# Kernel tuning notes

Measured on AMD Instinct MI355X. Metric: run time of the kernel, lower is better.

The kernel has to match this reference:

```python
import jax, jax.numpy as jnp
import numpy as np

B, H, S, D = 2, 16, 2048, 64
SCALE = D ** -0.5  # head_dim^-0.5 with dim=1024, num_heads=16


def setup_inputs() -> dict:
    key = jax.random.key(0)
    kq, kk, kv = jax.random.split(key, 3)
    q = jax.random.normal(kq, (B, H, S, D), dtype=jnp.float32)
    k = jax.random.normal(kk, (B, H, S, D), dtype=jnp.float32)
    v = jax.random.normal(kv, (B, H, S, D), dtype=jnp.float32)
    # causal mask, broadcastable over batch and heads; 0 -> masked
    mask = jnp.tril(jnp.ones((S, S), dtype=jnp.int32))[None, None]
    return {"q": q, "k": k, "v": v, "mask": mask}


def reference(q, k, v, mask):
    # scores: [B, H, S, S]
    scores = jnp.einsum("bhqd,bhkd->bhqk", q, k) * SCALE
    scores = jnp.where(mask == 0, jnp.float32(-jnp.inf), scores)
    attn_weights = jax.nn.softmax(scores, axis=-1)
    # dropout p=0 / eval mode -> identity
    attn_output = jnp.einsum("bhqk,bhkd->bhqd", attn_weights, v)
    return attn_output, attn_weights
```

## Files before the change

kernel.cpp:

```cpp
#include <hip/hip_runtime.h>


#define S_LEN 2048
#define HD 64
#define NHEADS 32
#define NQT 32
#define ATT_SCALE 0.125f

typedef __bf16 bf16x8 __attribute__((ext_vector_type(8)));
typedef unsigned short u16x8 __attribute__((ext_vector_type(8)));
typedef float f32x4 __attribute__((ext_vector_type(4)));

__device__ __forceinline__ unsigned short f2bf(float f) {
  unsigned int u = __builtin_bit_cast(unsigned int, f);
  u += 0x7fffu + ((u >> 16) & 1u);
  return (unsigned short)(u >> 16);
}
__device__ __forceinline__ bf16x8 frag16(const unsigned short* p) {
  uint4 u = *reinterpret_cast<const uint4*>(p);
  return __builtin_bit_cast(bf16x8, u);
}
__device__ __forceinline__ bf16x8 cvt8(const float* p) {
  const float4 a = *reinterpret_cast<const float4*>(p);
  const float4 b = *reinterpret_cast<const float4*>(p + 4);
  u16x8 r;
  r[0] = f2bf(a.x); r[1] = f2bf(a.y); r[2] = f2bf(a.z); r[3] = f2bf(a.w);
  r[4] = f2bf(b.x); r[5] = f2bf(b.y); r[6] = f2bf(b.z); r[7] = f2bf(b.w);
  return __builtin_bit_cast(bf16x8, r);
}
__device__ __forceinline__ bf16x8 load8(const void* base, size_t off, bool isf32) {
  if (isf32) return cvt8(reinterpret_cast<const float*>(base) + off);
  return frag16(reinterpret_cast<const unsigned short*>(base) + off);
}
__device__ __forceinline__ bool sniff_f32(const void* q) {
  const int lane = threadIdx.x & 63;
  const unsigned int w = reinterpret_cast<const unsigned int*>(q)[lane];
  const unsigned int le = (w >> 7) & 0xFFu;
  const bool okb = (le == 0u) || (le >= 100u && le <= 140u);
  return __popcll(__ballot(okb)) < 32;
}

__global__ __launch_bounds__(256) void prep_kernel(
    const void* __restrict__ q, const void* __restrict__ k, const void* __restrict__ v,
    unsigned short* __restrict__ wq, unsigned short* __restrict__ wk,
    unsigned short* __restrict__ wv) {
  __shared__ __align__(16) unsigned short T[HD][72];
  const int tid = threadIdx.x;
  if (blockIdx.x >= 1024) {
    const bool isf32 = sniff_f32(q);
    const size_t i = ((size_t)(blockIdx.x - 1024) * 256 + tid) * 8;
    bf16x8 a = load8(q, i, isf32);
    *reinterpret_cast<uint4*>(wq + i) = __builtin_bit_cast(uint4, a);
    bf16x8 b = load8(k, i, isf32);
    *reinterpret_cast<uint4*>(wk + i) = __builtin_bit_cast(uint4, b);
    return;
  }
  const bool isf32 = sniff_f32(v);
  const int head = blockIdx.x & (NHEADS - 1);
  const int tt = blockIdx.x >> 5;
  const int r = tid >> 2;
  const int dc = (tid & 3) << 4;
  const size_t off = ((size_t)head * S_LEN + (tt << 6) + r) * HD + dc;
  const bf16x8 x0 = load8(v, off, isf32);
  const bf16x8 x1 = load8(v, off + 8, isf32);
  const u16x8 e0 = __builtin_bit_cast(u16x8, x0);
  const u16x8 e1 = __builtin_bit_cast(u16x8, x1);
#pragma unroll
  for (int e = 0; e < 8; ++e) { T[dc + e][r] = e0[e]; T[dc + 8 + e][r] = e1[e]; }
  __syncthreads();
  const int d = tid >> 2;
  const int tc = (tid & 3) << 4;
  const uint4 o0 = *reinterpret_cast<const uint4*>(&T[d][tc]);
  const uint4 o1 = *reinterpret_cast<const uint4*>(&T[d][tc + 8]);
  unsigned short* dst = wv + (((size_t)(head * NQT + tt) * HD + d) << 6) + tc;
  *reinterpret_cast<uint4*>(dst) = o0;
  *reinterpret_cast<uint4*>(dst + 8) = o1;
}

template <bool WS>
__global__ __launch_bounds__(256, 4) void attn_kernel(
    const void* __restrict__ q, const void* __restrict__ kk, const void* __restrict__ vv,
    const unsigned short* __restrict__ wq, const unsigned short* __restrict__ wk,
    const unsigned short* __restrict__ wv,
    float* __restrict__ out_o, float* __restrict__ out_w) {
  __shared__ __align__(16) unsigned short Vt[WS ? 8 : 2 * HD * 72];

  const int blk = blockIdx.x;
  const int head = blk & (NHEADS - 1);
  const int qt = (NQT - 1) - (blk >> 5);
  const int tid = threadIdx.x;
  const int lane = tid & 63;
  const int wave = tid >> 6;
  const int q0 = qt << 6;
  const int r0 = q0 + (wave << 4);
  const int l15 = lane & 15;
  const int quad = lane >> 4;

  bool isf32 = true;
  if constexpr (!WS) isf32 = sniff_f32(q);

  const size_t qb = (size_t)head * S_LEN * HD;
  float* Wh = out_w + (size_t)head * S_LEN * S_LEN;

  {
    const int c0 = (qt + 1) << 6;
    const int nz4 = (S_LEN - c0) >> 2;
    const int row = tid >> 2;
    const f32x4 z = {0.f, 0.f, 0.f, 0.f};
    f32x4* wrow = reinterpret_cast<f32x4*>(Wh + (size_t)(q0 + row) * S_LEN + c0);
    for (int c = tid & 3; c < nz4; c += 4) __builtin_nontemporal_store(z, wrow + c);
  }

  const size_t qoff = qb + (size_t)(r0 + l15) * HD + (quad << 3);
  bf16x8 qa0, qa1;
  if constexpr (WS) { qa0 = frag16(wq + qoff); qa1 = frag16(wq + qoff + 32); }
  else              { qa0 = load8(q, qoff, isf32); qa1 = load8(q, qoff + 32, isf32); }

  const int krow_l = ((l15 >> 2) << 3) + (l15 & 3);
  auto ldk = [&](int kt, int f) -> bf16x8 {
    const int s = f >> 1;
    const int row = (kt << 6) + krow_l + ((s & 1) << 2) + ((s >> 1) << 5);
    const size_t o = qb + (size_t)row * HD + (quad << 3) + ((f & 1) << 5);
    if constexpr (WS) return frag16(wk + o);
    else return load8(kk, o, isf32);
  };
  const int kib_base = (quad << 3);
  const int qi = r0 + l15;

  float lsum = 0.f;
  {
    bf16x8 kc[8], kn[8];
#pragma unroll
    for (int f = 0; f < 8; ++f) kc[f] = ldk(0, f);
    for (int kt = 0; kt <= qt; ++kt) {
      if (kt < qt) {
#pragma unroll
        for (int f = 0; f < 8; ++f) kn[f] = ldk(kt + 1, f);
      }
      if (kt == qt) {
#pragma unroll
        for (int s = 0; s < 4; ++s) {
          f32x4 acc = {0.f, 0.f, 0.f, 0.f};
          acc = __builtin_amdgcn_mfma_f32_16x16x32_bf16(kc[2 * s], qa0, acc, 0, 0, 0);
          acc = __builtin_amdgcn_mfma_f32_16x16x32_bf16(kc[2 * s + 1], qa1, acc, 0, 0, 0);
          const int kib = (kt << 6) + kib_base + ((s & 1) << 2) + ((s >> 1) << 5);
#pragma unroll
          for (int r = 0; r < 4; ++r)
            lsum += (kib + r <= qi) ? __expf(acc[r] * ATT_SCALE) : 0.f;
        }
      } else {
#pragma unroll
        for (int s = 0; s < 4; ++s) {
          f32x4 acc = {0.f, 0.f, 0.f, 0.f};
          acc = __builtin_amdgcn_mfma_f32_16x16x32_bf16(kc[2 * s], qa0, acc, 0, 0, 0);
          acc = __builtin_amdgcn_mfma_f32_16x16x32_bf16(kc[2 * s + 1], qa1, acc, 0, 0, 0);
#pragma unroll
          for (int r = 0; r < 4; ++r) lsum += __expf(acc[r] * ATT_SCALE);
        }
#pragma unroll
        for (int f = 0; f < 8; ++f) kc[f] = kn[f];
      }
    }
  }
  lsum += __shfl_xor(lsum, 16);
  lsum += __shfl_xor(lsum, 32);
  const float inv_l = 1.0f / lsum;

  const f32x4 vzero = {0.f, 0.f, 0.f, 0.f};
  f32x4 oacc[4] = {vzero, vzero, vzero, vzero};

  if constexpr (WS) {
    const unsigned short* wvh = wv + ((size_t)(head * NQT) << 12);
    for (int kt = 0; kt <= qt; ++kt) {
      const bool last = (kt == qt);
      bf16x8 kf[8];
#pragma unroll
      for (int f = 0; f < 8; ++f) kf[f] = ldk(kt, f);
      bf16x8 vf[8];
      {
        const unsigned short* tb = wvh + ((size_t)kt << 12);
#pragma unroll
        for (int nc2 = 0; nc2 < 4; ++nc2) {
          const unsigned short* rp = tb + (((nc2 << 4) + l15) << 6) + (quad << 3);
          vf[2 * nc2] = frag16(rp);
          vf[2 * nc2 + 1] = frag16(rp + 32);
        }
      }

      float pb[4][4];
#pragma unroll
      for (int s = 0; s < 4; ++s) {
        f32x4 acc = {0.f, 0.f, 0.f, 0.f};
        acc = __builtin_amdgcn_mfma_f32_16x16x32_bf16(kf[2 * s], qa0, acc, 0, 0, 0);
        acc = __builtin_amdgcn_mfma_f32_16x16x32_bf16(kf[2 * s + 1], qa1, acc, 0, 0, 0);
        const int kib = (kt << 6) + kib_base + ((s & 1) << 2) + ((s >> 1) << 5);
        f32x4 pv;
#pragma unroll
        for (int r = 0; r < 4; ++r) {
          float p = __expf(acc[r] * ATT_SCALE) * inv_l;
          if (last) p = (kib + r <= qi) ? p : 0.f;
          pb[s][r] = p;
          pv[r] = p;
        }
        __builtin_nontemporal_store(
            pv, reinterpret_cast<f32x4*>(Wh + (size_t)qi * S_LEN + kib));
      }
      u16x8 a0, a1;
#pragma unroll
      for (int r = 0; r < 4; ++r) {
        a0[r] = f2bf(pb[0][r]); a0[4 + r] = f2bf(pb[1][r]);
        a1[r] = f2bf(pb[2][r]); a1[4 + r] = f2bf(pb[3][r]);
      }
      const bf16x8 pa0 = __builtin_bit_cast(bf16x8, a0);
      const bf16x8 pa1 = __builtin_bit_cast(bf16x8, a1);
#pragma unroll
      for (int nc2 = 0; nc2 < 4; ++nc2) {
        oacc[nc2] = __builtin_amdgcn_mfma_f32_16x16x32_bf16(pa0, vf[2 * nc2], oacc[nc2], 0, 0, 0);
        oacc[nc2] = __builtin_amdgcn_mfma_f32_16x16x32_bf16(pa1, vf[2 * nc2 + 1], oacc[nc2], 0, 0, 0);
      }
    }
  } else {
    const int ftr1 = tid >> 3, fdc = (tid & 7) << 3;
    const int ftr2 = (tid + 256) >> 3;
    bf16x8 fv0, fv1;
    auto vload = [&](int kt) {
      fv0 = load8(vv, qb + (size_t)((kt << 6) + ftr1) * HD + fdc, isf32);
      fv1 = load8(vv, qb + (size_t)((kt << 6) + ftr2) * HD + fdc, isf32);
    };
    auto vstage = [&](int buf) {
      const u16x8 s0 = __builtin_bit_cast(u16x8, fv0);
      const u16x8 s1 = __builtin_bit_cast(u16x8, fv1);
      const int tb1 = ftr1 >> 3, tl1 = ftr1 & 7;
      const int tb2 = ftr2 >> 3, tl2 = ftr2 & 7;
      unsigned short* Vb = &Vt[buf * HD * 72];
#pragma unroll
      for (int e = 0; e < 8; ++e) {
        const int d = fdc + e;
        Vb[d * 72 + (((tb1 ^ (d >> 3)) << 3) | tl1)] = s0[e];
        Vb[d * 72 + (((tb2 ^ (d >> 3)) << 3) | tl2)] = s1[e];
      }
    };
    vload(0);
    vstage(0);
    __syncthreads();
    for (int kt = 0; kt <= qt; ++kt) {
      const bool last = (kt == qt);
      bf16x8 kf[8];
#pragma unroll
      for (int f = 0; f < 8; ++f) kf[f] = ldk(kt, f);
      if (!last) vload(kt + 1);

      float pb[4][4];
#pragma unroll
      for (int s = 0; s < 4; ++s) {
        f32x4 acc = {0.f, 0.f, 0.f, 0.f};
        acc = __builtin_amdgcn_mfma_f32_16x16x32_bf16(kf[2 * s], qa0, acc, 0, 0, 0);
        acc = __builtin_amdgcn_mfma_f32_16x16x32_bf16(kf[2 * s + 1], qa1, acc, 0, 0, 0);
        const int kib = (kt << 6) + kib_base + ((s & 1) << 2) + ((s >> 1) << 5);
        f32x4 pv;
#pragma unroll
        for (int r = 0; r < 4; ++r) {
          float p = __expf(acc[r] * ATT_SCALE) * inv_l;
          if (last) p = (kib + r <= qi) ? p : 0.f;
          pb[s][r] = p;
          pv[r] = p;
        }
        __builtin_nontemporal_store(
            pv, reinterpret_cast<f32x4*>(Wh + (size_t)qi * S_LEN + kib));
      }
      u16x8 a0, a1;
#pragma unroll
      for (int r = 0; r < 4; ++r) {
        a0[r] = f2bf(pb[0][r]); a0[4 + r] = f2bf(pb[1][r]);
        a1[r] = f2bf(pb[2][r]); a1[4 + r] = f2bf(pb[3][r]);
      }
      const bf16x8 pa0 = __builtin_bit_cast(bf16x8, a0);
      const bf16x8 pa1 = __builtin_bit_cast(bf16x8, a1);
      const unsigned short* Vc = &Vt[(kt & 1) * HD * 72];
#pragma unroll
      for (int nc2 = 0; nc2 < 4; ++nc2) {
        const int n = (nc2 << 4) + l15;
        const unsigned short* vbp = Vc + n * 72;
        const int nb = n >> 3;
        const bf16x8 v0 = frag16(vbp + ((quad ^ nb) << 3));
        const bf16x8 v1 = frag16(vbp + (((4 + quad) ^ nb) << 3));
        oacc[nc2] = __builtin_amdgcn_mfma_f32_16x16x32_bf16(pa0, v0, oacc[nc2], 0, 0, 0);
        oacc[nc2] = __builtin_amdgcn_mfma_f32_16x16x32_bf16(pa1, v1, oacc[nc2], 0, 0, 0);
      }
      if (!last) {
        vstage((kt + 1) & 1);
        __syncthreads();
      }
    }
  }

#pragma unroll
  for (int nc2 = 0; nc2 < 4; ++nc2)
#pragma unroll
    for (int r = 0; r < 4; ++r)
      out_o[(size_t)(head * S_LEN + r0 + (quad << 2) + r) * HD + (nc2 << 4) + l15] =
          oacc[nc2][r];
}

extern "C" void kernel_launch(void* const* d_in, const int* in_sizes, int n_in,
                              void* d_out, int out_size, void* d_ws, size_t ws_size,
                              hipStream_t stream) {
  (void)in_sizes; (void)n_in; (void)out_size;
  const void* q = d_in[0];
  const void* k = d_in[1];
  const void* v = d_in[2];
  float* out = (float*)d_out;
  float* out_o = out;
  float* out_w = out + (size_t)NHEADS * S_LEN * HD;
  const size_t NE = (size_t)NHEADS * S_LEN * HD;
  if (d_ws && ws_size >= NE * 2 * 3) {
    unsigned short* wq = reinterpret_cast<unsigned short*>(d_ws);
    unsigned short* wk = wq + NE;
    unsigned short* wv = wk + NE;
    prep_kernel<<<dim3(1024 + NE / (256 * 8)), dim3(256), 0, stream>>>(q, k, v, wq, wk, wv);
    attn_kernel<true><<<dim3(NHEADS * NQT), dim3(256), 0, stream>>>(
        q, k, v, wq, wk, wv, out_o, out_w);
  } else {
    attn_kernel<false><<<dim3(NHEADS * NQT), dim3(256), 0, stream>>>(
        q, k, v, nullptr, nullptr, nullptr, out_o, out_w);
  }
}
```

Measured before the change: 779.6 us.

## Stage swizzled K/V tiles through double-buffered LDS in workspace attention kernel

The prep kernel now writes K and V in per-64-row tiles with an XOR swizzle. The workspace attention kernel cooperatively loads each K/V tile into double-buffered shared memory and reads MFMA fragments from LDS. Before, every wave loaded its own fragments straight from global memory. The change is meant to cut redundant global and L2 traffic across the four waves and to avoid LDS bank conflicts. It also moves zero-filling of the masked region to after the compute, and switches the attention-weight stores from nontemporal to regular stores, which may raise cache pollution and adds barriers per tile.

New measurement: 634.4 us. -18.6%, faster.

```diff
diff --git a/kernel.cpp b/kernel.cpp
--- a/kernel.cpp
+++ b/kernel.cpp
@@ -39,6 +39,7 @@
   const bool okb = (le == 0u) || (le >= 100u && le <= 140u);
   return __popcll(__ballot(okb)) < 32;
 }
+__device__ __forceinline__ int swz3(int r) { return (r & 3) | (((r >> 3) & 1) << 2); }
 
 __global__ __launch_bounds__(256) void prep_kernel(
     const void* __restrict__ q, const void* __restrict__ k, const void* __restrict__ v,
@@ -52,7 +53,14 @@
     bf16x8 a = load8(q, i, isf32);
     *reinterpret_cast<uint4*>(wq + i) = __builtin_bit_cast(uint4, a);
     bf16x8 b = load8(k, i, isf32);
-    *reinterpret_cast<uint4*>(wk + i) = __builtin_bit_cast(uint4, b);
+    const int d0 = (int)(i & 63);
+    const int t = (int)((i >> 6) & (S_LEN - 1));
+    const int head = (int)(i >> 17);
+    const int tl = t & 63;
+    const int sch = (d0 >> 3) ^ swz3(tl);
+    unsigned short* dst =
+        wk + (((size_t)(head << 5) + (t >> 6)) << 12) + tl * 64 + (sch << 3);
+    *reinterpret_cast<uint4*>(dst) = __builtin_bit_cast(uint4, b);
     return;
   }
   const bool isf32 = sniff_f32(v);
@@ -70,20 +78,20 @@
   __syncthreads();
   const int d = tid >> 2;
   const int tc = (tid & 3) << 4;
-  const uint4 o0 = *reinterpret_cast<const uint4*>(&T[d][tc]);
-  const uint4 o1 = *reinterpret_cast<const uint4*>(&T[d][tc + 8]);
-  unsigned short* dst = wv + (((size_t)(head * NQT + tt) * HD + d) << 6) + tc;
-  *reinterpret_cast<uint4*>(dst) = o0;
-  *reinterpret_cast<uint4*>(dst + 8) = o1;
-}
-
-template <bool WS>
-__global__ __launch_bounds__(256, 4) void attn_kernel(
-    const void* __restrict__ q, const void* __restrict__ kk, const void* __restrict__ vv,
+  const int c0 = tc >> 3;
+  unsigned short* base = wv + (((size_t)(head << 5) + tt) << 12) + d * 64;
+  *reinterpret_cast<uint4*>(base + ((c0 ^ swz3(d)) << 3)) =
+      *reinterpret_cast<const uint4*>(&T[d][tc]);
+  *reinterpret_cast<uint4*>(base + (((c0 + 1) ^ swz3(d)) << 3)) =
+      *reinterpret_cast<const uint4*>(&T[d][tc + 8]);
+}
+
+__global__ __launch_bounds__(256, 4) void attn_ws(
     const unsigned short* __restrict__ wq, const unsigned short* __restrict__ wk,
     const unsigned short* __restrict__ wv,
     float* __restrict__ out_o, float* __restrict__ out_w) {
-  __shared__ __align__(16) unsigned short Vt[WS ? 8 : 2 * HD * 72];
+  __shared__ __align__(16) unsigned short Kl[2][4096];
+  __shared__ __align__(16) unsigned short Vl[2][4096];
 
   const int blk = blockIdx.x;
   const int head = blk & (NHEADS - 1);
@@ -95,9 +103,157 @@
   const int r0 = q0 + (wave << 4);
   const int l15 = lane & 15;
   const int quad = lane >> 4;
-
-  bool isf32 = true;
-  if constexpr (!WS) isf32 = sniff_f32(q);
+  const int kswz = (l15 & 3) | (((l15 >> 2) & 1) << 2);
+  const int vswz = (l15 & 3) | (((l15 >> 3) & 1) << 2);
+  const int krow_l = ((l15 >> 2) << 3) + (l15 & 3);
+  const int qi = r0 + l15;
+
+  float* Wh = out_w + (size_t)head * S_LEN * S_LEN;
+  const unsigned short* wkh = wk + ((size_t)head << 17);
+  const unsigned short* wvh = wv + ((size_t)head << 17);
+
+  const size_t qoff = ((size_t)head << 17) + (size_t)(r0 + l15) * HD + (quad << 3);
+  const bf16x8 qa0 = frag16(wq + qoff);
+  const bf16x8 qa1 = frag16(wq + qoff + 32);
+
+  const int so = wave * 1024 + lane * 8;
+  uint4 sk0, sk1, sv0, sv1;
+  auto ldKg = [&](int kt) {
+    const unsigned short* p = wkh + ((size_t)kt << 12) + so;
+    sk0 = *reinterpret_cast<const uint4*>(p);
+    sk1 = *reinterpret_cast<const uint4*>(p + 512);
+  };
+  auto wrK = [&](int b) {
+    unsigned short* p = &Kl[b][so];
+    *reinterpret_cast<uint4*>(p) = sk0;
+    *reinterpret_cast<uint4*>(p + 512) = sk1;
+  };
+  auto ldVg = [&](int kt) {
+    const unsigned short* p = wvh + ((size_t)kt << 12) + so;
+    sv0 = *reinterpret_cast<const uint4*>(p);
+    sv1 = *reinterpret_cast<const uint4*>(p + 512);
+  };
+  auto wrV = [&](int b) {
+    unsigned short* p = &Vl[b][so];
+    *reinterpret_cast<uint4*>(p) = sv0;
+    *reinterpret_cast<uint4*>(p + 512) = sv1;
+  };
+
+  float lsum = 0.f;
+  ldKg(0); wrK(0); __syncthreads();
+  for (int kt = 0; kt <= qt; ++kt) {
+    if (kt < qt) ldKg(kt + 1);
+    const unsigned short* Kb = &Kl[kt & 1][0];
+#pragma unroll
+    for (int s = 0; s < 4; ++s) {
+      const int R = krow_l + ((s & 1) << 2) + ((s >> 1) << 5);
+      const unsigned short* rb = Kb + R * 64;
+      const bf16x8 k0 = frag16(rb + ((quad ^ kswz) << 3));
+      const bf16x8 k1 = frag16(rb + (((4 + quad) ^ kswz) << 3));
+      f32x4 acc = {0.f, 0.f, 0.f, 0.f};
+      acc = __builtin_amdgcn_mfma_f32_16x16x32_bf16(k0, qa0, acc, 0, 0, 0);
+      acc = __builtin_amdgcn_mfma_f32_16x16x32_bf16(k1, qa1, acc, 0, 0, 0);
+      if (kt == qt) {
+        const int kib = (kt << 6) + (quad << 3) + ((s & 1) << 2) + ((s >> 1) << 5);
+#pragma unroll
+        for (int r = 0; r < 4; ++r)
+          lsum += (kib + r <= qi) ? __expf(acc[r] * ATT_SCALE) : 0.f;
+      } else {
+#pragma unroll
+        for (int r = 0; r < 4; ++r) lsum += __expf(acc[r] * ATT_SCALE);
+      }
+    }
+    if (kt < qt) { wrK((kt + 1) & 1); __syncthreads(); }
+  }
+  lsum += __shfl_xor(lsum, 16);
+  lsum += __shfl_xor(lsum, 32);
+  const float inv_l = 1.0f / lsum;
+  __syncthreads();
+
+  const f32x4 vz = {0.f, 0.f, 0.f, 0.f};
+  f32x4 oacc[4] = {vz, vz, vz, vz};
+  ldKg(0); ldVg(0); wrK(0); wrV(0); __syncthreads();
+  for (int kt = 0; kt <= qt; ++kt) {
+    const bool last = (kt == qt);
+    if (!last) { ldKg(kt + 1); ldVg(kt + 1); }
+    const unsigned short* Kb = &Kl[kt & 1][0];
+    const unsigned short* Vb = &Vl[kt & 1][0];
+
+    float pb[4][4];
+#pragma unroll
+    for (int s = 0; s < 4; ++s) {
+      const int R = krow_l + ((s & 1) << 2) + ((s >> 1) << 5);
+      const unsigned short* rb = Kb + R * 64;
+      const bf16x8 k0 = frag16(rb + ((quad ^ kswz) << 3));
+      const bf16x8 k1 = frag16(rb + (((4 + quad) ^ kswz) << 3));
+      f32x4 acc = {0.f, 0.f, 0.f, 0.f};
+      acc = __builtin_amdgcn_mfma_f32_16x16x32_bf16(k0, qa0, acc, 0, 0, 0);
+      acc = __builtin_amdgcn_mfma_f32_16x16x32_bf16(k1, qa1, acc, 0, 0, 0);
+      const int kib = (kt << 6) + (quad << 3) + ((s & 1) << 2) + ((s >> 1) << 5);
+      f32x4 pv;
+#pragma unroll
+      for (int r = 0; r < 4; ++r) {
+        float p = __expf(acc[r] * ATT_SCALE) * inv_l;
+        if (last) p = (kib + r <= qi) ? p : 0.f;
+        pb[s][r] = p;
+        pv[r] = p;
+      }
+      *reinterpret_cast<f32x4*>(Wh + (size_t)qi * S_LEN + kib) = pv;
+    }
+    u16x8 a0, a1;
+#pragma unroll
+    for (int r = 0; r < 4; ++r) {
+      a0[r] = f2bf(pb[0][r]); a0[4 + r] = f2bf(pb[1][r]);
+      a1[r] = f2bf(pb[2][r]); a1[4 + r] = f2bf(pb[3][r]);
+    }
+    const bf16x8 pa0 = __builtin_bit_cast(bf16x8, a0);
+    const bf16x8 pa1 = __builtin_bit_cast(bf16x8, a1);
+#pragma unroll
+    for (int nc2 = 0; nc2 < 4; ++nc2) {
+      const unsigned short* rb = Vb + ((nc2 << 4) + l15) * 64;
+      const bf16x8 v0 = frag16(rb + ((quad ^ vswz) << 3));
+      const bf16x8 v1 = frag16(rb + (((4 + quad) ^ vswz) << 3));
+      oacc[nc2] = __builtin_amdgcn_mfma_f32_16x16x32_bf16(pa0, v0, oacc[nc2], 0, 0, 0);
+      oacc[nc2] = __builtin_amdgcn_mfma_f32_16x16x32_bf16(pa1, v1, oacc[nc2], 0, 0, 0);
+    }
+    if (!last) { wrK((kt + 1) & 1); wrV((kt + 1) & 1); __syncthreads(); }
+  }
+
+#pragma unroll
+  for (int nc2 = 0; nc2 < 4; ++nc2)
+#pragma unroll
+    for (int r = 0; r < 4; ++r)
+      out_o[(size_t)(head * S_LEN + r0 + (quad << 2) + r) * HD + (nc2 << 4) + l15] =
+          oacc[nc2][r];
+
+  {
+    const int c0 = (qt + 1) << 6;
+    const f32x4 z = {0.f, 0.f, 0.f, 0.f};
+#pragma unroll 1
+    for (int rr = 0; rr < 16; ++rr) {
+      float* rowp = Wh + (size_t)(r0 + rr) * S_LEN;
+      for (int c = c0 + (lane << 2); c < S_LEN; c += 256)
+        __builtin_nontemporal_store(z, reinterpret_cast<f32x4*>(rowp + c));
+    }
+  }
+}
+
+__global__ __launch_bounds__(256, 4) void attn_fb(
+    const void* __restrict__ q, const void* __restrict__ kk, const void* __restrict__ vv,
+    float* __restrict__ out_o, float* __restrict__ out_w) {
+  __shared__ __align__(16) unsigned short Vt[2 * HD * 72];
+
+  const int blk = blockIdx.x;
+  const int head = blk & (NHEADS - 1);
+  const int qt = (NQT - 1) - (blk >> 5);
+  const int tid = threadIdx.x;
+  const int lane = tid & 63;
+  const int wave = tid >> 6;
+  const int q0 = qt << 6;
+  const int r0 = q0 + (wave << 4);
+  const int l15 = lane & 15;
+  const int quad = lane >> 4;
+  const bool isf32 = sniff_f32(q);
 
   const size_t qb = (size_t)head * S_LEN * HD;
   float* Wh = out_w + (size_t)head * S_LEN * S_LEN;
@@ -108,21 +264,19 @@
     const int row = tid >> 2;
     const f32x4 z = {0.f, 0.f, 0.f, 0.f};
     f32x4* wrow = reinterpret_cast<f32x4*>(Wh + (size_t)(q0 + row) * S_LEN + c0);
-    for (int c = tid & 3; c < nz4; c += 4) __builtin_nontemporal_store(z, wrow + c);
+    for (int c = tid & 3; c < nz4; c += 4) wrow[c] = z;
   }
 
   const size_t qoff = qb + (size_t)(r0 + l15) * HD + (quad << 3);
-  bf16x8 qa0, qa1;
-  if constexpr (WS) { qa0 = frag16(wq + qoff); qa1 = frag16(wq + qoff + 32); }
-  else              { qa0 = load8(q, qoff, isf32); qa1 = load8(q, qoff + 32, isf32); }
+  const bf16x8 qa0 = load8(q, qoff, isf32);
+  const bf16x8 qa1 = load8(q, qoff + 32, isf32);
 
   const int krow_l = ((l15 >> 2) << 3) + (l15 & 3);
   auto ldk = [&](int kt, int f) -> bf16x8 {
     const int s = f >> 1;
     const int row = (kt << 6) + krow_l + ((s & 1) << 2) + ((s >> 1) << 5);
     const size_t o = qb + (size_t)row * HD + (quad << 3) + ((f & 1) << 5);
-    if constexpr (WS) return frag16(wk + o);
-    else return load8(kk, o, isf32);
+    return load8(kk, o, isf32);
   };
   const int kib_base = (quad << 3);
   const int qi = r0 + l15;
@@ -137,26 +291,17 @@
 #pragma unroll
         for (int f = 0; f < 8; ++f) kn[f] = ldk(kt + 1, f);
       }
-      if (kt == qt) {
-#pragma unroll
-        for (int s = 0; s < 4; ++s) {
-          f32x4 acc = {0.f, 0.f, 0.f, 0.f};
-          acc = __builtin_amdgcn_mfma_f32_16x16x32_bf16(kc[2 * s], qa0, acc, 0, 0, 0);
-          acc = __builtin_amdgcn_mfma_f32_16x16x32_bf16(kc[2 * s + 1], qa1, acc, 0, 0, 0);
-          const int kib = (kt << 6) + kib_base + ((s & 1) << 2) + ((s >> 1) << 5);
-#pragma unroll
-          for (int r = 0; r < 4; ++r)
-            lsum += (kib + r <= qi) ? __expf(acc[r] * ATT_SCALE) : 0.f;
-        }
-      } else {
-#pragma unroll
-        for (int s = 0; s < 4; ++s) {
-          f32x4 acc = {0.f, 0.f, 0.f, 0.f};
-          acc = __builtin_amdgcn_mfma_f32_16x16x32_bf16(kc[2 * s], qa0, acc, 0, 0, 0);
-          acc = __builtin_amdgcn_mfma_f32_16x16x32_bf16(kc[2 * s + 1], qa1, acc, 0, 0, 0);
-#pragma unroll
-          for (int r = 0; r < 4; ++r) lsum += __expf(acc[r] * ATT_SCALE);
-        }
+#pragma unroll
+      for (int s = 0; s < 4; ++s) {
+        f32x4 acc = {0.f, 0.f, 0.f, 0.f};
+        acc = __builtin_amdgcn_mfma_f32_16x16x32_bf16(kc[2 * s], qa0, acc, 0, 0, 0);
+        acc = __builtin_amdgcn_mfma_f32_16x16x32_bf16(kc[2 * s + 1], qa1, acc, 0, 0, 0);
+        const int kib = (kt << 6) + kib_base + ((s & 1) << 2) + ((s >> 1) << 5);
+#pragma unroll
+        for (int r = 0; r < 4; ++r)
+          lsum += (kt < qt || kib + r <= qi) ? __expf(acc[r] * ATT_SCALE) : 0.f;
+      }
+      if (kt < qt) {
 #pragma unroll
         for (int f = 0; f < 8; ++f) kc[f] = kn[f];
       }
@@ -166,131 +311,78 @@
   lsum += __shfl_xor(lsum, 32);
   const float inv_l = 1.0f / lsum;
 
-  const f32x4 vzero = {0.f, 0.f, 0.f, 0.f};
-  f32x4 oacc[4] = {vzero, vzero, vzero, vzero};
-
-  if constexpr (WS) {
-    const unsigned short* wvh = wv + ((size_t)(head * NQT) << 12);
-    for (int kt = 0; kt <= qt; ++kt) {
-      const bool last = (kt == qt);
-      bf16x8 kf[8];
-#pragma unroll
-      for (int f = 0; f < 8; ++f) kf[f] = ldk(kt, f);
-      bf16x8 vf[8];
-      {
-        const unsigned short* tb = wvh + ((size_t)kt << 12);
-#pragma unroll
-        for (int nc2 = 0; nc2 < 4; ++nc2) {
-          const unsigned short* rp = tb + (((nc2 << 4) + l15) << 6) + (quad << 3);
-          vf[2 * nc2] = frag16(rp);
-          vf[2 * nc2 + 1] = frag16(rp + 32);
-        }
-      }
-
-      float pb[4][4];
-#pragma unroll
-      for (int s = 0; s < 4; ++s) {
-        f32x4 acc = {0.f, 0.f, 0.f, 0.f};
-        acc = __builtin_amdgcn_mfma_f32_16x16x32_bf16(kf[2 * s], qa0, acc, 0, 0, 0);
-        acc = __builtin_amdgcn_mfma_f32_16x16x32_bf16(kf[2 * s + 1], qa1, acc, 0, 0, 0);
-        const int kib = (kt << 6) + kib_base + ((s & 1) << 2) + ((s >> 1) << 5);
-        f32x4 pv;
-#pragma unroll
-        for (int r = 0; r < 4; ++r) {
-          float p = __expf(acc[r] * ATT_SCALE) * inv_l;
-          if (last) p = (kib + r <= qi) ? p : 0.f;
-          pb[s][r] = p;
-          pv[r] = p;
-        }
-        __builtin_nontemporal_store(
-            pv, reinterpret_cast<f32x4*>(Wh + (size_t)qi * S_LEN + kib));
-      }
-      u16x8 a0, a1;
+  const f32x4 vz = {0.f, 0.f, 0.f, 0.f};
+  f32x4 oacc[4] = {vz, vz, vz, vz};
+
+  const int ftr1 = tid >> 3, fdc = (tid & 7) << 3;
+  const int ftr2 = (tid + 256) >> 3;
+  bf16x8 fv0, fv1;
+  auto vload = [&](int kt) {
+    fv0 = load8(vv, qb + (size_t)((kt << 6) + ftr1) * HD + fdc, isf32);
+    fv1 = load8(vv, qb + (size_t)((kt << 6) + ftr2) * HD + fdc, isf32);
+  };
+  auto vstage = [&](int buf) {
+    const u16x8 s0 = __builtin_bit_cast(u16x8, fv0);
+    const u16x8 s1 = __builtin_bit_cast(u16x8, fv1);
+    const int tb1 = ftr1 >> 3, tl1 = ftr1 & 7;
+    const int tb2 = ftr2 >> 3, tl2 = ftr2 & 7;
+    unsigned short* Vb = &Vt[buf * HD * 72];
+#pragma unroll
+    for (int e = 0; e < 8; ++e) {
+      const int d = fdc + e;
+      Vb[d * 72 + (((tb1 ^ (d >> 3)) << 3) | tl1)] = s0[e];
+      Vb[d * 72 + (((tb2 ^ (d >> 3)) << 3) | tl2)] = s1[e];
+    }
+  };
+  vload(0);
+  vstage(0);
+  __syncthreads();
+  for (int kt = 0; kt <= qt; ++kt) {
+    const bool last = (kt == qt);
+    bf16x8 kf[8];
+#pragma unroll
+    for (int f = 0; f < 8; ++f) kf[f] = ldk(kt, f);
+    if (!last) vload(kt + 1);
+
+    float pb[4][4];
+#pragma unroll
+    for (int s = 0; s < 4; ++s) {
+      f32x4 acc = {0.f, 0.f, 0.f, 0.f};
+      acc = __builtin_amdgcn_mfma_f32_16x16x32_bf16(kf[2 * s], qa0, acc, 0, 0, 0);
+      acc = __builtin_amdgcn_mfma_f32_16x16x32_bf16(kf[2 * s + 1], qa1, acc, 0, 0, 0);
+      const int kib = (kt << 6) + kib_base + ((s & 1) << 2) + ((s >> 1) << 5);
+      f32x4 pv;
 #pragma unroll
       for (int r = 0; r < 4; ++r) {
-        a0[r] = f2bf(pb[0][r]); a0[4 + r] = f2bf(pb[1][r]);
-        a1[r] = f2bf(pb[2][r]); a1[4 + r] = f2bf(pb[3][r]);
-      }
-      const bf16x8 pa0 = __builtin_bit_cast(bf16x8, a0);
-      const bf16x8 pa1 = __builtin_bit_cast(bf16x8, a1);
-#pragma unroll
-      for (int nc2 = 0; nc2 < 4; ++nc2) {
-        oacc[nc2] = __builtin_amdgcn_mfma_f32_16x16x32_bf16(pa0, vf[2 * nc2], oacc[nc2], 0, 0, 0);
-        oacc[nc2] = __builtin_amdgcn_mfma_f32_16x16x32_bf16(pa1, vf[2 * nc2 + 1], oacc[nc2], 0, 0, 0);
-      }
-    }
-  } else {
-    const int ftr1 = tid >> 3, fdc = (tid & 7) << 3;
-    const int ftr2 = (tid + 256) >> 3;
-    bf16x8 fv0, fv1;
-    auto vload = [&](int kt) {
-      fv0 = load8(vv, qb + (size_t)((kt << 6) + ftr1) * HD + fdc, isf32);
-      fv1 = load8(vv, qb + (size_t)((kt << 6) + ftr2) * HD + fdc, isf32);
-    };
-    auto vstage = [&](int buf) {
-      const u16x8 s0 = __builtin_bit_cast(u16x8, fv0);
-      const u16x8 s1 = __builtin_bit_cast(u16x8, fv1);
-      const int tb1 = ftr1 >> 3, tl1 = ftr1 & 7;
-      const int tb2 = ftr2 >> 3, tl2 = ftr2 & 7;
-      unsigned short* Vb = &Vt[buf * HD * 72];
-#pragma unroll
-      for (int e = 0; e < 8; ++e) {
-        const int d = fdc + e;
-        Vb[d * 72 + (((tb1 ^ (d >> 3)) << 3) | tl1)] = s0[e];
-        Vb[d * 72 + (((tb2 ^ (d >> 3)) << 3) | tl2)] = s1[e];
-      }
-    };
-    vload(0);
-    vstage(0);
-    __syncthreads();
-    for (int kt = 0; kt <= qt; ++kt) {
-      const bool last = (kt == qt);
-      bf16x8 kf[8];
-#pragma unroll
-      for (int f = 0; f < 8; ++f) kf[f] = ldk(kt, f);
-      if (!last) vload(kt + 1);
-
-      float pb[4][4];
-#pragma unroll
-      for (int s = 0; s < 4; ++s) {
-        f32x4 acc = {0.f, 0.f, 0.f, 0.f};
-        acc = __builtin_amdgcn_mfma_f32_16x16x32_bf16(kf[2 * s], qa0, acc, 0, 0, 0);
-        acc = __builtin_amdgcn_mfma_f32_16x16x32_bf16(kf[2 * s + 1], qa1, acc, 0, 0, 0);
-        const int kib = (kt << 6) + kib_base + ((s & 1) << 2) + ((s >> 1) << 5);
-        f32x4 pv;
-#pragma unroll
-        for (int r = 0; r < 4; ++r) {
-          float p = __expf(acc[r] * ATT_SCALE) * inv_l;
-          if (last) p = (kib + r <= qi) ? p : 0.f;
-          pb[s][r] = p;
-          pv[r] = p;
-        }
-        __builtin_nontemporal_store(
-            pv, reinterpret_cast<f32x4*>(Wh + (size_t)qi * S_LEN + kib));
-      }
-      u16x8 a0, a1;
-#pragma unroll
-      for (int r = 0; r < 4; ++r) {
-        a0[r] = f2bf(pb[0][r]); a0[4 + r] = f2bf(pb[1][r]);
-        a1[r] = f2bf(pb[2][r]); a1[4 + r] = f2bf(pb[3][r]);
-      }
-      const bf16x8 pa0 = __builtin_bit_cast(bf16x8, a0);
-      const bf16x8 pa1 = __builtin_bit_cast(bf16x8, a1);
-      const unsigned short* Vc = &Vt[(kt & 1) * HD * 72];
-#pragma unroll
-      for (int nc2 = 0; nc2 < 4; ++nc2) {
-        const int n = (nc2 << 4) + l15;
-        const unsigned short* vbp = Vc + n * 72;
-        const int nb = n >> 3;
-        const bf16x8 v0 = frag16(vbp + ((quad ^ nb) << 3));
-        const bf16x8 v1 = frag16(vbp + (((4 + quad) ^ nb) << 3));
-        oacc[nc2] = __builtin_amdgcn_mfma_f32_16x16x32_bf16(pa0, v0, oacc[nc2], 0, 0, 0);
-        oacc[nc2] = __builtin_amdgcn_mfma_f32_16x16x32_bf16(pa1, v1, oacc[nc2], 0, 0, 0);
-      }
-      if (!last) {
-        vstage((kt + 1) & 1);
-        __syncthreads();
-      }
+        float p = __expf(acc[r] * ATT_SCALE) * inv_l;
+        if (last) p = (kib + r <= qi) ? p : 0.f;
+        pb[s][r] = p;
+        pv[r] = p;
+      }
+      *reinterpret_cast<f32x4*>(Wh + (size_t)qi * S_LEN + kib) = pv;
+    }
+    u16x8 a0, a1;
+#pragma unroll
+    for (int r = 0; r < 4; ++r) {
+      a0[r] = f2bf(pb[0][r]); a0[4 + r] = f2bf(pb[1][r]);
+      a1[r] = f2bf(pb[2][r]); a1[4 + r] = f2bf(pb[3][r]);
+    }
+    const bf16x8 pa0 = __builtin_bit_cast(bf16x8, a0);
+    const bf16x8 pa1 = __builtin_bit_cast(bf16x8, a1);
+    const unsigned short* Vc = &Vt[(kt & 1) * HD * 72];
+#pragma unroll
+    for (int nc2 = 0; nc2 < 4; ++nc2) {
+      const int n = (nc2 << 4) + l15;
+      const unsigned short* vbp = Vc + n * 72;
+      const int nb = n >> 3;
+      const bf16x8 v0 = frag16(vbp + ((quad ^ nb) << 3));
+      const bf16x8 v1 = frag16(vbp + (((4 + quad) ^ nb) << 3));
+      oacc[nc2] = __builtin_amdgcn_mfma_f32_16x16x32_bf16(pa0, v0, oacc[nc2], 0, 0, 0);
+      oacc[nc2] = __builtin_amdgcn_mfma_f32_16x16x32_bf16(pa1, v1, oacc[nc2], 0, 0, 0);
+    }
+    if (!last) {
+      vstage((kt + 1) & 1);
+      __syncthreads();
     }
   }
 
@@ -318,10 +410,8 @@
     unsigned short* wk = wq + NE;
     unsigned short* wv = wk + NE;
     prep_kernel<<<dim3(1024 + NE / (256 * 8)), dim3(256), 0, stream>>>(q, k, v, wq, wk, wv);
-    attn_kernel<true><<<dim3(NHEADS * NQT), dim3(256), 0, stream>>>(
-        q, k, v, wq, wk, wv, out_o, out_w);
+    attn_ws<<<dim3(NHEADS * NQT), dim3(256), 0, stream>>>(wq, wk, wv, out_o, out_w);
   } else {
-    attn_kernel<false><<<dim3(NHEADS * NQT), dim3(256), 0, stream>>>(
-        q, k, v, nullptr, nullptr, nullptr, out_o, out_w);
-  }
-}
+    attn_fb<<<dim3(NHEADS * NQT), dim3(256), 0, stream>>>(q, k, v, out_o, out_w);
+  }
+}
```
